# Kernel optimization log

Hardware: AMD Instinct MI355X
Metric: run time of the kernel (lower is better)

Reference implementation:

```python
import jax, jax.numpy as jnp
import numpy as np

B, S, H, T = 64, 512, 768, 9


def setup_inputs() -> dict:
    key = jax.random.key(0)
    ks = jax.random.split(key, 8)
    embeddings = jax.random.normal(ks[0], (B, S, H), dtype=jnp.float32)
    # variable-length mask (first token always valid), as token_type_ids would give
    lengths = jax.random.randint(ks[1], (B,), 1, S + 1)
    mask = (jnp.arange(S)[None, :] < lengths[:, None]).astype(jnp.int32)
    labels = jax.random.randint(ks[2], (B, S), 0, T)
    W = jax.random.normal(ks[3], (T, H), dtype=jnp.float32) * (1.0 / np.sqrt(H))
    b = jnp.zeros((T,), dtype=jnp.float32)
    start_trans = jax.random.normal(ks[4], (T,), dtype=jnp.float32) * 0.1
    transitions = jax.random.normal(ks[5], (T, T), dtype=jnp.float32) * 0.1
    end_trans = jax.random.normal(ks[6], (T,), dtype=jnp.float32) * 0.1
    return {"embeddings": embeddings, "W": W, "b": b,
            "start_trans": start_trans, "transitions": transitions,
            "end_trans": end_trans, "labels": labels, "mask": mask}


def _crf_nll(emissions, labels, mask_bool, start_trans, transitions, end_trans):
    # emissions: [B,S,T]; returns negative log-likelihood per sequence [B]
    Bn = emissions.shape[0]
    mask_f = mask_bool.astype(emissions.dtype)
    # --- gold path score (numerator) ---
    first = start_trans[labels[:, 0]] + emissions[jnp.arange(Bn), 0, labels[:, 0]]
    emis_sc = jnp.take_along_axis(emissions, labels[..., None], axis=2)[..., 0]  # [B,S]
    trans_sc = transitions[labels[:, :-1], labels[:, 1:]]                         # [B,S-1]
    num = first + jnp.sum((emis_sc[:, 1:] + trans_sc) * mask_f[:, 1:], axis=1)
    last_idx = jnp.sum(mask_bool.astype(jnp.int32), axis=1) - 1
    last_lab = jnp.take_along_axis(labels, last_idx[:, None], axis=1)[:, 0]
    num = num + end_trans[last_lab]
    # --- log partition (forward algorithm, logsumexp recurrence) ---
    alpha0 = start_trans[None, :] + emissions[:, 0]          # [B,T]
    em_t = jnp.swapaxes(emissions, 0, 1)[1:]                 # [S-1,B,T]
    m_t = mask_bool.T[1:]                                    # [S-1,B]
    def step(alpha, xs):
        em, m = xs
        new = jax.nn.logsumexp(alpha[:, :, None] + transitions[None], axis=1) + em
        return jnp.where(m[:, None], new, alpha), None
    alpha, _ = jax.lax.scan(step, alpha0, (em_t, m_t))
    denom = jax.nn.logsumexp(alpha + end_trans[None, :], axis=1)
    return denom - num


def reference(embeddings, W, b, start_trans, transitions, end_trans, labels, mask):
    # dropout is identity at eval; Linear + ReLU emissions
    emissions = jax.nn.relu(jnp.einsum('bsh,th->bst', embeddings, W) + b)
    # -100 padding handling: zero out mask there, clamp labels to 0
    valid = labels != -100
    mask_bool = (mask != 0) & valid
    labels_mod = jnp.where(valid, labels, 0)
    nll = _crf_nll(emissions, labels_mod, mask_bool, start_trans, transitions, end_trans)
    return jnp.mean(nll)  # == -loss.mean() of the log-likelihood
```

## Files before the change

kernel.cpp:

```cpp
#include <hip/hip_runtime.h>

#define NEG_INF (-1e30f)

static constexpr int Bn = 64;
static constexpr int Sn = 512;
static constexpr int Hn = 768;
static constexpr int Tn = 9;
static constexpr int KC = 32;
static constexpr int CL = 16;

__device__ __forceinline__ float dot4(float4 a, float4 b) {
    return a.x * b.x + a.y * b.y + a.z * b.z + a.w * b.w;
}

__global__ __launch_bounds__(256) void emis_kernel(const float* __restrict__ emb,
        const float* __restrict__ Wm, const float* __restrict__ bias,
        float* __restrict__ em) {
    const int lane = threadIdx.x & 63;
    const int gwave = (blockIdx.x * 256 + threadIdx.x) >> 6;
    const int nwaves = gridDim.x * 4;

    float4 w[Tn][3];
#pragma unroll
    for (int t = 0; t < Tn; ++t) {
        const float4* w4 = (const float4*)(Wm + t * Hn);
#pragma unroll
        for (int i = 0; i < 3; ++i) w[t][i] = w4[lane + (i << 6)];
    }
    float bb[Tn];
#pragma unroll
    for (int t = 0; t < Tn; ++t) bb[t] = bias[t];

    for (int row = gwave; row < Bn * Sn; row += nwaves) {
        const float4* e4 = (const float4*)(emb + (size_t)row * Hn);
        float4 e0 = e4[lane];
        float4 e1 = e4[lane + 64];
        float4 e2 = e4[lane + 128];
        float acc[Tn];
#pragma unroll
        for (int t = 0; t < Tn; ++t)
            acc[t] = dot4(e0, w[t][0]) + dot4(e1, w[t][1]) + dot4(e2, w[t][2]);
#pragma unroll
        for (int t = 0; t < Tn; ++t) {
#pragma unroll
            for (int off = 32; off; off >>= 1)
                acc[t] += __shfl_xor(acc[t], off);
        }
        if (lane == 0) {
#pragma unroll
            for (int t = 0; t < Tn; ++t)
                em[(size_t)row * Tn + t] = fmaxf(acc[t] + bb[t], 0.0f);
        }
    }
}

__global__ __launch_bounds__(128) void chunk_kernel(const float* __restrict__ em,
        const float* __restrict__ trans, const int* __restrict__ labels,
        const int* __restrict__ mask, float* __restrict__ chunkM) {
    const int bk = blockIdx.x;
    const int b = bk >> 5;
    const int k = bk & 31;
    const int tid = threadIdx.x;
    const int i = tid / 9;
    const int j = tid - i * 9;
    const int t0 = 1 + k * CL;

    __shared__ float P[2][81];
    __shared__ float em_s[CL * Tn];
    __shared__ int on_s[CL];

    {
        const int nst = (Sn - t0 < CL) ? (Sn - t0) : CL;
        const int base = (b * Sn + t0) * Tn;
        for (int u = tid; u < nst * Tn; u += 128) em_s[u] = em[base + u];
        if (tid < CL) {
            int t = t0 + tid;
            int on = 0;
            if (t < Sn)
                on = (mask[b * Sn + t] != 0) && (labels[b * Sn + t] != -100);
            on_s[tid] = on;
        }
    }

    float c[Tn];
    if (tid < 81) {
#pragma unroll
        for (int kk = 0; kk < Tn; ++kk) c[kk] = trans[kk * Tn + j];
        P[0][tid] = (i == j) ? 0.0f : NEG_INF;
    }
    __syncthreads();

    int cur = 0;
#pragma unroll
    for (int u = 0; u < CL; ++u) {
        if (!on_s[u]) continue;
        if (tid < 81) {
            float x[Tn];
#pragma unroll
            for (int kk = 0; kk < Tn; ++kk) x[kk] = P[cur][i * 9 + kk] + c[kk];
            float mx = x[0];
#pragma unroll
            for (int kk = 1; kk < Tn; ++kk) mx = fmaxf(mx, x[kk]);
            float s = 0.0f;
#pragma unroll
            for (int kk = 0; kk < Tn; ++kk) s += __expf(x[kk] - mx);
            P[cur ^ 1][tid] = mx + __logf(s) + em_s[u * Tn + j];
        }
        __syncthreads();
        cur ^= 1;
    }
    if (tid < 81) chunkM[(size_t)bk * 81 + tid] = P[cur][tid];
}

__global__ __launch_bounds__(64) void combine_kernel(const float* __restrict__ em,
        const float* __restrict__ chunkM, const float* __restrict__ startT,
        const float* __restrict__ trans, const float* __restrict__ endT,
        const int* __restrict__ labels, const int* __restrict__ mask,
        float* __restrict__ nll) {
    const int b = blockIdx.x;
    const int lane = threadIdx.x;

    float alpha = NEG_INF;
    if (lane < Tn) alpha = startT[lane] + em[((size_t)b * Sn) * Tn + lane];

    for (int k = 0; k < KC; ++k) {
        const float* P = chunkM + ((size_t)b * KC + k) * 81;
        float a[Tn];
#pragma unroll
        for (int i = 0; i < Tn; ++i) a[i] = __shfl(alpha, i);
        float na = NEG_INF;
        if (lane < Tn) {
            float x[Tn];
#pragma unroll
            for (int i = 0; i < Tn; ++i) x[i] = a[i] + P[i * Tn + lane];
            float mx = x[0];
#pragma unroll
            for (int i = 1; i < Tn; ++i) mx = fmaxf(mx, x[i]);
            float s = 0.0f;
#pragma unroll
            for (int i = 0; i < Tn; ++i) s += __expf(x[i] - mx);
            na = mx + __logf(s);
        }
        alpha = na;
    }

    float z = (lane < Tn) ? (alpha + endT[lane]) : NEG_INF;
    float mx = z;
#pragma unroll
    for (int off = 32; off; off >>= 1) mx = fmaxf(mx, __shfl_xor(mx, off));
    float s = __expf(z - mx);
#pragma unroll
    for (int off = 32; off; off >>= 1) s += __shfl_xor(s, off);
    float denom = mx + __logf(s);

    float nump = 0.0f;
    int cnt = 0;
    for (int t = lane; t < Sn; t += 64) {
        int m = mask[b * Sn + t];
        int lab = labels[b * Sn + t];
        bool valid = (lab != -100);
        bool mb = (m != 0) && valid;
        cnt += mb ? 1 : 0;
        if (t >= 1 && mb) {
            int labm = valid ? lab : 0;
            int labp = labels[b * Sn + t - 1];
            labp = (labp != -100) ? labp : 0;
            nump += em[((size_t)b * Sn + t) * Tn + labm] + trans[labp * Tn + labm];
        }
    }
#pragma unroll
    for (int off = 32; off; off >>= 1) {
        nump += __shfl_xor(nump, off);
        cnt += __shfl_xor(cnt, off);
    }

    if (lane == 0) {
        int lab0 = labels[b * Sn];
        lab0 = (lab0 != -100) ? lab0 : 0;
        float first = startT[lab0] + em[((size_t)b * Sn) * Tn + lab0];
        int lastIdx = cnt - 1;
        if (lastIdx < 0) lastIdx = 0;
        int lastLab = labels[b * Sn + lastIdx];
        lastLab = (lastLab != -100) ? lastLab : 0;
        float num = first + nump + endT[lastLab];
        nll[b] = denom - num;
    }
}

__global__ __launch_bounds__(64) void mean_kernel(const float* __restrict__ nll,
        float* __restrict__ out) {
    float v = nll[threadIdx.x];
#pragma unroll
    for (int off = 32; off; off >>= 1) v += __shfl_xor(v, off);
    if (threadIdx.x == 0) out[0] = v * (1.0f / 64.0f);
}

extern "C" void kernel_launch(void* const* d_in, const int* in_sizes, int n_in,
                              void* d_out, int out_size, void* d_ws, size_t ws_size,
                              hipStream_t stream) {
    const float* emb    = (const float*)d_in[0];
    const float* Wm     = (const float*)d_in[1];
    const float* bias   = (const float*)d_in[2];
    const float* startT = (const float*)d_in[3];
    const float* trans  = (const float*)d_in[4];
    const float* endT   = (const float*)d_in[5];
    const int*   labels = (const int*)d_in[6];
    const int*   mask   = (const int*)d_in[7];

    float* em     = (float*)d_ws;
    float* chunkM = em + (size_t)Bn * Sn * Tn;
    float* nll    = chunkM + (size_t)Bn * KC * 81;
    float* out    = (float*)d_out;

    emis_kernel<<<768, 256, 0, stream>>>(emb, Wm, bias, em);
    chunk_kernel<<<Bn * KC, 128, 0, stream>>>(em, trans, labels, mask, chunkM);
    combine_kernel<<<Bn, 64, 0, stream>>>(em, chunkM, startT, trans, endT, labels, mask, nll);
    mean_kernel<<<1, 64, 0, stream>>>(nll, out);
}
```

Before: 64.97 us.

## Fuse emission GEMV into chunked CRF scan and move gold-path scoring into chunks

Each chunk block now computes its own 16 emission rows straight from the embeddings, so the separate emission kernel and the global emission buffer go away. The 9x9 chunk scan runs in wave registers using shuffles (two waves split the rows) instead of double-buffered shared memory with a block barrier per step. The gold-path partial sums and counts are also computed per chunk, and the combine kernel recomputes emission row 0 and prefetches transposed, padded chunk matrices as float4. Each block reloads the full W matrix (27 float4 per lane), which raises register pressure and redundant W reads across 2048 blocks.

```diff
diff --git a/kernel.cpp b/kernel.cpp
--- a/kernel.cpp
+++ b/kernel.cpp
@@ -8,140 +8,215 @@
 static constexpr int Tn = 9;
 static constexpr int KC = 32;
 static constexpr int CL = 16;
+static constexpr int PSTRIDE = 108;
 
 __device__ __forceinline__ float dot4(float4 a, float4 b) {
     return a.x * b.x + a.y * b.y + a.z * b.z + a.w * b.w;
 }
 
-__global__ __launch_bounds__(256) void emis_kernel(const float* __restrict__ emb,
-        const float* __restrict__ Wm, const float* __restrict__ bias,
-        float* __restrict__ em) {
-    const int lane = threadIdx.x & 63;
-    const int gwave = (blockIdx.x * 256 + threadIdx.x) >> 6;
-    const int nwaves = gridDim.x * 4;
-
-    float4 w[Tn][3];
+__global__ __launch_bounds__(128) void fused_chunk_kernel(
+        const float* __restrict__ emb, const float* __restrict__ Wm,
+        const float* __restrict__ bias, const float* __restrict__ trans,
+        const int* __restrict__ labels, const int* __restrict__ mask,
+        float* __restrict__ chunkP, float* __restrict__ auxN,
+        int* __restrict__ auxC) {
+    const int bk = blockIdx.x;
+    const int b  = bk >> 5;
+    const int k  = bk & 31;
+    const int t0 = 1 + k * CL;
+    const int tid  = threadIdx.x;
+    const int w    = tid >> 6;
+    const int lane = tid & 63;
+
+    __shared__ float em_s[CL][Tn];
+    __shared__ int   on_s[CL];
+    __shared__ float tr_s[81];
+
+    float4 wr[Tn][3];
 #pragma unroll
     for (int t = 0; t < Tn; ++t) {
         const float4* w4 = (const float4*)(Wm + t * Hn);
 #pragma unroll
-        for (int i = 0; i < 3; ++i) w[t][i] = w4[lane + (i << 6)];
+        for (int i = 0; i < 3; ++i) wr[t][i] = w4[lane + (i << 6)];
     }
     float bb[Tn];
 #pragma unroll
     for (int t = 0; t < Tn; ++t) bb[t] = bias[t];
 
-    for (int row = gwave; row < Bn * Sn; row += nwaves) {
-        const float4* e4 = (const float4*)(emb + (size_t)row * Hn);
+    if (tid < 81) tr_s[tid] = trans[tid];
+
+    int myLab = 0, myLabP = 0, myOn = 0;
+    if (tid < CL) {
+        int t = t0 + tid;
+        if (t < Sn) {
+            int lb = labels[b * Sn + t];
+            int lp = labels[b * Sn + t - 1];
+            int mm = mask[b * Sn + t];
+            myOn  = (mm != 0) && (lb != -100);
+            myLab = (lb == -100) ? 0 : lb;
+            myLabP = (lp == -100) ? 0 : lp;
+        }
+        on_s[tid] = myOn;
+    }
+
+#pragma unroll
+    for (int rr = 0; rr < 8; ++rr) {
+        const int r = w * 8 + rr;
+        const int t = t0 + r;
+        const int trow = (t < Sn) ? t : (Sn - 1);
+        const float4* e4 = (const float4*)(emb + ((size_t)b * Sn + trow) * Hn);
         float4 e0 = e4[lane];
         float4 e1 = e4[lane + 64];
         float4 e2 = e4[lane + 128];
         float acc[Tn];
 #pragma unroll
-        for (int t = 0; t < Tn; ++t)
-            acc[t] = dot4(e0, w[t][0]) + dot4(e1, w[t][1]) + dot4(e2, w[t][2]);
-#pragma unroll
-        for (int t = 0; t < Tn; ++t) {
+        for (int t9 = 0; t9 < Tn; ++t9)
+            acc[t9] = dot4(e0, wr[t9][0]) + dot4(e1, wr[t9][1]) + dot4(e2, wr[t9][2]);
+#pragma unroll
+        for (int t9 = 0; t9 < Tn; ++t9) {
 #pragma unroll
             for (int off = 32; off; off >>= 1)
-                acc[t] += __shfl_xor(acc[t], off);
+                acc[t9] += __shfl_xor(acc[t9], off);
         }
         if (lane == 0) {
 #pragma unroll
-            for (int t = 0; t < Tn; ++t)
-                em[(size_t)row * Tn + t] = fmaxf(acc[t] + bb[t], 0.0f);
-        }
-    }
-}
-
-__global__ __launch_bounds__(128) void chunk_kernel(const float* __restrict__ em,
-        const float* __restrict__ trans, const int* __restrict__ labels,
-        const int* __restrict__ mask, float* __restrict__ chunkM) {
-    const int bk = blockIdx.x;
-    const int b = bk >> 5;
-    const int k = bk & 31;
-    const int tid = threadIdx.x;
-    const int i = tid / 9;
-    const int j = tid - i * 9;
-    const int t0 = 1 + k * CL;
-
-    __shared__ float P[2][81];
-    __shared__ float em_s[CL * Tn];
-    __shared__ int on_s[CL];
-
-    {
-        const int nst = (Sn - t0 < CL) ? (Sn - t0) : CL;
-        const int base = (b * Sn + t0) * Tn;
-        for (int u = tid; u < nst * Tn; u += 128) em_s[u] = em[base + u];
-        if (tid < CL) {
-            int t = t0 + tid;
-            int on = 0;
-            if (t < Sn)
-                on = (mask[b * Sn + t] != 0) && (labels[b * Sn + t] != -100);
-            on_s[tid] = on;
-        }
-    }
+            for (int t9 = 0; t9 < Tn; ++t9)
+                em_s[r][t9] = fmaxf(acc[t9] + bb[t9], 0.0f);
+        }
+    }
+    __syncthreads();
+
+    float nump = 0.0f;
+    int cnt = 0;
+    if (tid < CL && myOn) {
+        nump = em_s[tid][myLab] + tr_s[myLabP * Tn + myLab];
+        cnt = 1;
+    }
+    if (w == 0) {
+#pragma unroll
+        for (int off = 8; off; off >>= 1) {
+            nump += __shfl_xor(nump, off);
+            cnt  += __shfl_xor(cnt, off);
+        }
+        if (lane == 0) { auxN[bk] = nump; auxC[bk] = cnt; }
+    }
+
+    const int v  = lane / 9;
+    const int jj = lane - v * 9;
+    const bool act = lane < ((w == 0) ? 45 : 36);
+    const int rid = (w == 0) ? v : (5 + v);
 
     float c[Tn];
-    if (tid < 81) {
-#pragma unroll
-        for (int kk = 0; kk < Tn; ++kk) c[kk] = trans[kk * Tn + j];
-        P[0][tid] = (i == j) ? 0.0f : NEG_INF;
-    }
-    __syncthreads();
-
-    int cur = 0;
-#pragma unroll
+#pragma unroll
+    for (int kk = 0; kk < Tn; ++kk) c[kk] = tr_s[kk * Tn + jj];
+
+    float pv = (act && rid == jj) ? 0.0f : NEG_INF;
+
     for (int u = 0; u < CL; ++u) {
         if (!on_s[u]) continue;
-        if (tid < 81) {
-            float x[Tn];
-#pragma unroll
-            for (int kk = 0; kk < Tn; ++kk) x[kk] = P[cur][i * 9 + kk] + c[kk];
-            float mx = x[0];
-#pragma unroll
-            for (int kk = 1; kk < Tn; ++kk) mx = fmaxf(mx, x[kk]);
-            float s = 0.0f;
-#pragma unroll
-            for (int kk = 0; kk < Tn; ++kk) s += __expf(x[kk] - mx);
-            P[cur ^ 1][tid] = mx + __logf(s) + em_s[u * Tn + j];
-        }
-        __syncthreads();
-        cur ^= 1;
-    }
-    if (tid < 81) chunkM[(size_t)bk * 81 + tid] = P[cur][tid];
-}
-
-__global__ __launch_bounds__(64) void combine_kernel(const float* __restrict__ em,
-        const float* __restrict__ chunkM, const float* __restrict__ startT,
-        const float* __restrict__ trans, const float* __restrict__ endT,
-        const int* __restrict__ labels, const int* __restrict__ mask,
+        float x[Tn];
+#pragma unroll
+        for (int kk = 0; kk < Tn; ++kk) {
+            float a = __shfl(pv, (v * Tn + kk) & 63);
+            x[kk] = a + c[kk];
+        }
+        float mx = x[0];
+#pragma unroll
+        for (int kk = 1; kk < Tn; ++kk) mx = fmaxf(mx, x[kk]);
+        float s = 0.0f;
+#pragma unroll
+        for (int kk = 0; kk < Tn; ++kk) s += __expf(x[kk] - mx);
+        float nv = mx + __logf(s) + em_s[u][jj];
+        pv = act ? nv : pv;
+    }
+    if (act) chunkP[(size_t)bk * PSTRIDE + jj * 12 + rid] = pv;
+}
+
+__global__ __launch_bounds__(64) void combine_kernel(
+        const float* __restrict__ emb, const float* __restrict__ Wm,
+        const float* __restrict__ bias, const float* __restrict__ startT,
+        const float* __restrict__ endT, const int* __restrict__ labels,
+        const int* __restrict__ mask, const float* __restrict__ chunkP,
+        const float* __restrict__ auxN, const int* __restrict__ auxC,
         float* __restrict__ nll) {
     const int b = blockIdx.x;
     const int lane = threadIdx.x;
 
-    float alpha = NEG_INF;
-    if (lane < Tn) alpha = startT[lane] + em[((size_t)b * Sn) * Tn + lane];
-
+    float4 wr[Tn][3];
+#pragma unroll
+    for (int t = 0; t < Tn; ++t) {
+        const float4* w4 = (const float4*)(Wm + t * Hn);
+#pragma unroll
+        for (int i = 0; i < 3; ++i) wr[t][i] = w4[lane + (i << 6)];
+    }
+    const float4* e4 = (const float4*)(emb + (size_t)b * Sn * Hn);
+    float4 e0 = e4[lane];
+    float4 e1 = e4[lane + 64];
+    float4 e2 = e4[lane + 128];
+    float acc[Tn];
+#pragma unroll
+    for (int t = 0; t < Tn; ++t)
+        acc[t] = dot4(e0, wr[t][0]) + dot4(e1, wr[t][1]) + dot4(e2, wr[t][2]);
+#pragma unroll
+    for (int t = 0; t < Tn; ++t) {
+#pragma unroll
+        for (int off = 32; off; off >>= 1)
+            acc[t] += __shfl_xor(acc[t], off);
+    }
+    float em0 = NEG_INF;
+#pragma unroll
+    for (int t = 0; t < Tn; ++t) {
+        float vt = fmaxf(acc[t] + bias[t], 0.0f);
+        if (lane == t) em0 = vt;
+    }
+    float alpha = (lane < Tn) ? (startT[lane] + em0) : NEG_INF;
+
+    int lab0r = labels[b * Sn];
+    int lab0 = (lab0r == -100) ? 0 : lab0r;
+    float first = startT[lab0] + __shfl(em0, lab0);
+
+    float numP = (lane < KC) ? auxN[b * KC + lane] : 0.0f;
+    int   cntP = (lane < KC) ? auxC[b * KC + lane] : 0;
+#pragma unroll
+    for (int off = 32; off; off >>= 1) {
+        numP += __shfl_xor(numP, off);
+        cntP += __shfl_xor(cntP, off);
+    }
+    int m0 = ((mask[b * Sn] != 0) && (lab0r != -100)) ? 1 : 0;
+    int cntTot = cntP + m0;
+    int lastIdx = cntTot - 1;
+    if (lastIdx < 0) lastIdx = 0;
+    int lastLab = labels[b * Sn + lastIdx];
+    lastLab = (lastLab == -100) ? 0 : lastLab;
+    float num = first + numP + endT[lastLab];
+
+    const float* Pb = chunkP + (size_t)b * KC * PSTRIDE;
+    float4 p0 = make_float4(0, 0, 0, 0), p1 = p0, p2 = p0;
+    if (lane < Tn) {
+        const float4* pp = (const float4*)(Pb + lane * 12);
+        p0 = pp[0]; p1 = pp[1]; p2 = pp[2];
+    }
     for (int k = 0; k < KC; ++k) {
-        const float* P = chunkM + ((size_t)b * KC + k) * 81;
-        float a[Tn];
-#pragma unroll
-        for (int i = 0; i < Tn; ++i) a[i] = __shfl(alpha, i);
-        float na = NEG_INF;
-        if (lane < Tn) {
-            float x[Tn];
-#pragma unroll
-            for (int i = 0; i < Tn; ++i) x[i] = a[i] + P[i * Tn + lane];
-            float mx = x[0];
-#pragma unroll
-            for (int i = 1; i < Tn; ++i) mx = fmaxf(mx, x[i]);
-            float s = 0.0f;
-#pragma unroll
-            for (int i = 0; i < Tn; ++i) s += __expf(x[i] - mx);
-            na = mx + __logf(s);
-        }
-        alpha = na;
+        float4 q0 = p0, q1 = p1, q2 = p2;
+        if (k + 1 < KC && lane < Tn) {
+            const float4* pp = (const float4*)(Pb + (size_t)(k + 1) * PSTRIDE + lane * 12);
+            p0 = pp[0]; p1 = pp[1]; p2 = pp[2];
+        }
+        float av[Tn];
+#pragma unroll
+        for (int i = 0; i < Tn; ++i) av[i] = __shfl(alpha, i);
+        float x[Tn];
+        x[0] = av[0] + q0.x; x[1] = av[1] + q0.y; x[2] = av[2] + q0.z;
+        x[3] = av[3] + q0.w; x[4] = av[4] + q1.x; x[5] = av[5] + q1.y;
+        x[6] = av[6] + q1.z; x[7] = av[7] + q1.w; x[8] = av[8] + q2.x;
+        float mx = x[0];
+#pragma unroll
+        for (int i = 1; i < Tn; ++i) mx = fmaxf(mx, x[i]);
+        float s = 0.0f;
+#pragma unroll
+        for (int i = 0; i < Tn; ++i) s += __expf(x[i] - mx);
+        float na = mx + __logf(s);
+        alpha = (lane < Tn) ? na : NEG_INF;
     }
 
     float z = (lane < Tn) ? (alpha + endT[lane]) : NEG_INF;
@@ -153,38 +228,7 @@
     for (int off = 32; off; off >>= 1) s += __shfl_xor(s, off);
     float denom = mx + __logf(s);
 
-    float nump = 0.0f;
-    int cnt = 0;
-    for (int t = lane; t < Sn; t += 64) {
-        int m = mask[b * Sn + t];
-        int lab = labels[b * Sn + t];
-        bool valid = (lab != -100);
-        bool mb = (m != 0) && valid;
-        cnt += mb ? 1 : 0;
-        if (t >= 1 && mb) {
-            int labm = valid ? lab : 0;
-            int labp = labels[b * Sn + t - 1];
-            labp = (labp != -100) ? labp : 0;
-            nump += em[((size_t)b * Sn + t) * Tn + labm] + trans[labp * Tn + labm];
-        }
-    }
-#pragma unroll
-    for (int off = 32; off; off >>= 1) {
-        nump += __shfl_xor(nump, off);
-        cnt += __shfl_xor(cnt, off);
-    }
-
-    if (lane == 0) {
-        int lab0 = labels[b * Sn];
-        lab0 = (lab0 != -100) ? lab0 : 0;
-        float first = startT[lab0] + em[((size_t)b * Sn) * Tn + lab0];
-        int lastIdx = cnt - 1;
-        if (lastIdx < 0) lastIdx = 0;
-        int lastLab = labels[b * Sn + lastIdx];
-        lastLab = (lastLab != -100) ? lastLab : 0;
-        float num = first + nump + endT[lastLab];
-        nll[b] = denom - num;
-    }
+    if (lane == 0) nll[b] = denom - num;
 }
 
 __global__ __launch_bounds__(64) void mean_kernel(const float* __restrict__ nll,
@@ -207,13 +251,15 @@
     const int*   labels = (const int*)d_in[6];
     const int*   mask   = (const int*)d_in[7];
 
-    float* em     = (float*)d_ws;
-    float* chunkM = em + (size_t)Bn * Sn * Tn;
-    float* nll    = chunkM + (size_t)Bn * KC * 81;
+    float* chunkP = (float*)d_ws;
+    float* auxN   = chunkP + (size_t)Bn * KC * PSTRIDE;
+    int*   auxC   = (int*)(auxN + (size_t)Bn * KC);
+    float* nll    = (float*)(auxC + (size_t)Bn * KC);
     float* out    = (float*)d_out;
 
-    emis_kernel<<<768, 256, 0, stream>>>(emb, Wm, bias, em);
-    chunk_kernel<<<Bn * KC, 128, 0, stream>>>(em, trans, labels, mask, chunkM);
-    combine_kernel<<<Bn, 64, 0, stream>>>(em, chunkM, startT, trans, endT, labels, mask, nll);
+    fused_chunk_kernel<<<Bn * KC, 128, 0, stream>>>(emb, Wm, bias, trans,
+                                                    labels, mask, chunkP, auxN, auxC);
+    combine_kernel<<<Bn, 64, 0, stream>>>(emb, Wm, bias, startT, endT,
+                                          labels, mask, chunkP, auxN, auxC, nll);
     mean_kernel<<<1, 64, 0, stream>>>(nll, out);
 }
```

Result: faster. 61.05 us (-6.0%).
